# Kernel optimization log

Measured on AMD Instinct MI355X. Metric: run time of the kernel, lower is better.

Reference implementation:

```python
import jax, jax.numpy as jnp
import numpy as np

DIM_IN = 1024
DIM_OUT = 1024
B = 8192


def setup_inputs() -> dict:
    key = jax.random.key(0)
    ks = jax.random.split(key, 8)
    d = DIM_IN + DIM_OUT
    bound = 1.0 / np.sqrt(d)
    def lin(kw, kb):
        W = jax.random.uniform(kw, (d, DIM_OUT), jnp.float32, -bound, bound)
        b = jax.random.uniform(kb, (DIM_OUT,), jnp.float32, -bound, bound)
        return W, b
    kx, kh, kc, kp = ks[0], ks[1], ks[2], ks[3]
    pw = jax.random.split(kp, 8)
    W_I, b_I = lin(pw[0], pw[1])
    W_F, b_F = lin(pw[2], pw[3])
    W_G, b_G = lin(pw[4], pw[5])
    W_O, b_O = lin(pw[6], pw[7])
    return {
        "x": jax.random.normal(kx, (B, DIM_IN), jnp.float32),
        "h": jax.random.normal(kh, (B, DIM_OUT), jnp.float32),
        "c": jax.random.normal(kc, (B, DIM_OUT), jnp.float32),
        "W_I": W_I, "b_I": b_I,
        "W_F": W_F, "b_F": b_F,
        "W_G": W_G, "b_G": b_G,
        "W_O": W_O, "b_O": b_O,
    }


def reference(x, h, c, W_I, b_I, W_F, b_F, W_G, b_G, W_O, b_O):
    X = jnp.concatenate([x, h], axis=-1)  # [B, dimIn+dimOut]
    # Fuse the 4 gate projections into one GEMM: [B,d] @ [d, 4*dimOut]
    W = jnp.concatenate([W_I, W_F, W_G, W_O], axis=1)
    b = jnp.concatenate([b_I, b_F, b_G, b_O], axis=0)
    gates = X @ W + b
    i_, f_, g_, o_ = jnp.split(gates, 4, axis=-1)
    I = jax.nn.sigmoid(i_)
    F = jax.nn.sigmoid(f_)
    G = jnp.tanh(g_)
    O = jax.nn.sigmoid(o_)
    C = F * c + I * G
    return O * jnp.tanh(C), C
```

## Files before the change

kernel.cpp:

```cpp
#include <hip/hip_runtime.h>
#include <cstdint>


#define B_ROWS 8192
#define DK 2048
#define DOUT 1024
#define TM 128
#define TN 128
#define BK 32

typedef __bf16 bf16x8 __attribute__((ext_vector_type(8)));
typedef __bf16 bf16x4 __attribute__((ext_vector_type(4)));
typedef float f32x4 __attribute__((ext_vector_type(4)));

__device__ inline void load16_to_lds(const __bf16* gsrc, __bf16* ldst) {
    __builtin_amdgcn_global_load_lds(
        (const __attribute__((address_space(1))) void*)gsrc,
        (__attribute__((address_space(3))) void*)ldst,
        16, 0, 0);
}

__device__ inline float fast_sigmoid(float x) {
    return __builtin_amdgcn_rcpf(1.0f + __builtin_amdgcn_exp2f(-1.442695041f * x));
}
__device__ inline float fast_tanh(float x) {
    return 1.0f - 2.0f * __builtin_amdgcn_rcpf(1.0f + __builtin_amdgcn_exp2f(2.885390082f * x));
}

__global__ __launch_bounds__(256) void prep_x(const float* __restrict__ x,
                                              const float* __restrict__ h,
                                              __bf16* __restrict__ X) {
    int id = blockIdx.x * 256 + threadIdx.x;
    int b = id >> 9;
    int k = (id & 511) * 4;
    float4 v;
    if (k < 1024) v = *(const float4*)&x[(size_t)b * 1024 + k];
    else          v = *(const float4*)&h[(size_t)b * 1024 + (k - 1024)];
    bf16x4 o = { (__bf16)v.x, (__bf16)v.y, (__bf16)v.z, (__bf16)v.w };
    *(bf16x4*)&X[(size_t)b * 2048 + k] = o;
}

__global__ __launch_bounds__(256) void prep_w(const float* __restrict__ WI,
                                              const float* __restrict__ WF,
                                              const float* __restrict__ WG,
                                              const float* __restrict__ WO,
                                              __bf16* __restrict__ Wt) {
    int kb = blockIdx.x;
    int jb = blockIdx.y;
    int j0 = jb * 32;
    __shared__ float t[32][33];
    int tx = threadIdx.x, ty = threadIdx.y;
    const float* Ws[4] = {WI, WF, WG, WO};
#pragma unroll
    for (int g = 0; g < 4; ++g) {
        const float* W = Ws[g];
#pragma unroll
        for (int yy = 0; yy < 32; yy += 8) {
            int k = kb * 32 + ty + yy;
            t[ty + yy][tx] = W[(size_t)k * 1024 + j0 + tx];
        }
        __syncthreads();
#pragma unroll
        for (int yy = 0; yy < 32; yy += 8) {
            int r = ty + yy;
            int npp = (jb * 2 + (r >> 4)) * 64 + g * 16 + (r & 15);
            Wt[(size_t)npp * 2048 + kb * 32 + tx] = (__bf16)t[tx][r];
        }
        __syncthreads();
    }
}

__global__ __launch_bounds__(256) void lstm_gemm(
    const __bf16* __restrict__ Xbf, const __bf16* __restrict__ Wt,
    const float* __restrict__ c,
    const float* __restrict__ bI, const float* __restrict__ bF,
    const float* __restrict__ bG, const float* __restrict__ bO,
    float* __restrict__ outH, float* __restrict__ outC)
{
    __shared__ __bf16 As[TM * BK];
    __shared__ __bf16 Bs[TN * BK];

    const int t = threadIdx.x;
    const int lane = t & 63;
    const int wave = t >> 6;
    const int wm = wave >> 1;
    const int wn = wave & 1;
    const int m0 = blockIdx.x * TM;
    const int nb = blockIdx.y;
    const int n0 = nb * TN;

    f32x4 acc[4][4];
#pragma unroll
    for (int i = 0; i < 4; ++i)
#pragma unroll
        for (int j = 0; j < 4; ++j) acc[i][j] = (f32x4){0.f, 0.f, 0.f, 0.f};

    const int r0 = t >> 2, kc0 = (t & 3) * 8;
    const int r1 = 64 + r0;
    const __bf16* gA0 = Xbf + (size_t)(m0 + r0) * DK + kc0;
    const __bf16* gA1 = Xbf + (size_t)(m0 + r1) * DK + kc0;
    const __bf16* gB0 = Wt + (size_t)(n0 + r0) * DK + kc0;
    const __bf16* gB1 = Wt + (size_t)(n0 + r1) * DK + kc0;
    __bf16* lA0 = As + wave * 512;
    __bf16* lA1 = As + 2048 + wave * 512;
    __bf16* lB0 = Bs + wave * 512;
    __bf16* lB1 = Bs + 2048 + wave * 512;

    const int lr = lane & 15;
    const int kh = (lane >> 4) * 8;
    const int arow = wm * 64 + lr;
    const int brow = wn * 64 + lr;

    for (int kk = 0; kk < DK / BK; ++kk) {
        load16_to_lds(gA0, lA0);
        load16_to_lds(gA1, lA1);
        load16_to_lds(gB0, lB0);
        load16_to_lds(gB1, lB1);
        gA0 += BK; gA1 += BK; gB0 += BK; gB1 += BK;
        __syncthreads();

        bf16x8 a[4], b[4];
#pragma unroll
        for (int i = 0; i < 4; ++i)
            a[i] = *(const bf16x8*)&As[(arow + i * 16) * BK + kh];
#pragma unroll
        for (int j = 0; j < 4; ++j)
            b[j] = *(const bf16x8*)&Bs[(brow + j * 16) * BK + kh];
#pragma unroll
        for (int i = 0; i < 4; ++i)
#pragma unroll
            for (int j = 0; j < 4; ++j)
                acc[i][j] = __builtin_amdgcn_mfma_f32_16x16x32_bf16(a[i], b[j], acc[i][j], 0, 0, 0);
        __syncthreads();
    }

    const int col = lane & 15;
    const int j = (nb * 2 + wn) * 16 + col;
    const float biI = bI[j], biF = bF[j], biG = bG[j], biO = bO[j];
    const int rbase = m0 + wm * 64 + (lane >> 4) * 4;
#pragma unroll
    for (int i = 0; i < 4; ++i) {
#pragma unroll
        for (int r = 0; r < 4; ++r) {
            int row = rbase + i * 16 + r;
            float I = fast_sigmoid(acc[i][0][r] + biI);
            float F = fast_sigmoid(acc[i][1][r] + biF);
            float G = fast_tanh(acc[i][2][r] + biG);
            float O = fast_sigmoid(acc[i][3][r] + biO);
            size_t idx = (size_t)row * DOUT + j;
            float Cn = F * c[idx] + I * G;
            outH[idx] = O * fast_tanh(Cn);
            outC[idx] = Cn;
        }
    }
}

extern "C" void kernel_launch(void* const* d_in, const int* in_sizes, int n_in,
                              void* d_out, int out_size, void* d_ws, size_t ws_size,
                              hipStream_t stream) {
    const float* x  = (const float*)d_in[0];
    const float* h  = (const float*)d_in[1];
    const float* c  = (const float*)d_in[2];
    const float* WI = (const float*)d_in[3];
    const float* bI = (const float*)d_in[4];
    const float* WF = (const float*)d_in[5];
    const float* bF = (const float*)d_in[6];
    const float* WG = (const float*)d_in[7];
    const float* bG = (const float*)d_in[8];
    const float* WO = (const float*)d_in[9];
    const float* bO = (const float*)d_in[10];

    __bf16* Xbf = (__bf16*)d_ws;
    __bf16* Wt  = (__bf16*)((char*)d_ws + (size_t)B_ROWS * DK * 2);
    float* outH = (float*)d_out;
    float* outC = outH + (size_t)B_ROWS * DOUT;

    prep_x<<<(B_ROWS * DK / 4) / 256, 256, 0, stream>>>(x, h, Xbf);
    prep_w<<<dim3(DK / 32, DOUT / 32), dim3(32, 8), 0, stream>>>(WI, WF, WG, WO, Wt);
    lstm_gemm<<<dim3(B_ROWS / TM, 4 * DOUT / TN), 256, 0, stream>>>(
        Xbf, Wt, c, bI, bF, bG, bO, outH, outC);
}
```

Measured before the change: 359.6 us.

## Restructure LSTM GEMM into 256x256 double-buffered tiles with swizzled LDS

Rewrites the main GEMM to use 256x256 block tiles with 512 threads and a BK=64 K-step split into two halves. LDS is double-buffered so global-to-LDS loads for the next step overlap the MFMAs on the current one, using explicit waitcnt, barriers and setprio. The LDS layout is XOR-swizzled to avoid bank conflicts, and block IDs are remapped for better L2 locality. Each wave holds more accumulators (8x4), which raises register pressure and may reduce occupancy.

```diff
diff --git a/kernel.cpp b/kernel.cpp
--- a/kernel.cpp
+++ b/kernel.cpp
@@ -5,9 +5,10 @@
 #define B_ROWS 8192
 #define DK 2048
 #define DOUT 1024
-#define TM 128
-#define TN 128
-#define BK 32
+#define BM 256
+#define BN 256
+#define BK 64
+#define NKT (DK / BK)
 
 typedef __bf16 bf16x8 __attribute__((ext_vector_type(8)));
 typedef __bf16 bf16x4 __attribute__((ext_vector_type(4)));
@@ -70,83 +71,117 @@
     }
 }
 
-__global__ __launch_bounds__(256) void lstm_gemm(
+__global__ __launch_bounds__(512, 2) void lstm_gemm(
     const __bf16* __restrict__ Xbf, const __bf16* __restrict__ Wt,
     const float* __restrict__ c,
     const float* __restrict__ bI, const float* __restrict__ bF,
     const float* __restrict__ bG, const float* __restrict__ bO,
     float* __restrict__ outH, float* __restrict__ outC)
 {
-    __shared__ __bf16 As[TM * BK];
-    __shared__ __bf16 Bs[TN * BK];
-
-    const int t = threadIdx.x;
-    const int lane = t & 63;
-    const int wave = t >> 6;
-    const int wm = wave >> 1;
-    const int wn = wave & 1;
-    const int m0 = blockIdx.x * TM;
-    const int nb = blockIdx.y;
-    const int n0 = nb * TN;
-
-    f32x4 acc[4][4];
-#pragma unroll
-    for (int i = 0; i < 4; ++i)
-#pragma unroll
-        for (int j = 0; j < 4; ++j) acc[i][j] = (f32x4){0.f, 0.f, 0.f, 0.f};
-
-    const int r0 = t >> 2, kc0 = (t & 3) * 8;
-    const int r1 = 64 + r0;
-    const __bf16* gA0 = Xbf + (size_t)(m0 + r0) * DK + kc0;
-    const __bf16* gA1 = Xbf + (size_t)(m0 + r1) * DK + kc0;
-    const __bf16* gB0 = Wt + (size_t)(n0 + r0) * DK + kc0;
-    const __bf16* gB1 = Wt + (size_t)(n0 + r1) * DK + kc0;
-    __bf16* lA0 = As + wave * 512;
-    __bf16* lA1 = As + 2048 + wave * 512;
-    __bf16* lB0 = Bs + wave * 512;
-    __bf16* lB1 = Bs + 2048 + wave * 512;
+    __shared__ __bf16 lds[2][2][2][8192];
+
+    const int tid  = threadIdx.x;
+    const int lane = tid & 63;
+    const int wave = tid >> 6;
+    const int wm = wave >> 2;
+    const int wn = wave & 3;
+
+    const int bid = blockIdx.x;
+    const int id  = (bid & 7) * 64 + (bid >> 3);
+    const int mb = id & 31;
+    const int nb = id >> 5;
+    const int m0 = mb * BM;
+    const int n0 = nb * BN;
+
+    const int o0  = wave * 1024 + lane * 16;
+    const int r0  = o0 >> 6;
+    const int lc0 = ((o0 >> 4) & 3) ^ ((r0 >> 1) & 3);
+    const __bf16* gA0 = Xbf + (size_t)(m0 + r0)       * DK + lc0 * 8;
+    const __bf16* gA1 = Xbf + (size_t)(m0 + r0 + 128) * DK + lc0 * 8;
+    const __bf16* gB0 = Wt  + (size_t)(n0 + r0)       * DK + lc0 * 8;
+    const __bf16* gB1 = Wt  + (size_t)(n0 + r0 + 128) * DK + lc0 * 8;
+    const int ls0 = wave * 512;
+    const int ls1 = ls0 + 4096;
 
     const int lr = lane & 15;
-    const int kh = (lane >> 4) * 8;
-    const int arow = wm * 64 + lr;
-    const int brow = wn * 64 + lr;
-
-    for (int kk = 0; kk < DK / BK; ++kk) {
-        load16_to_lds(gA0, lA0);
-        load16_to_lds(gA1, lA1);
-        load16_to_lds(gB0, lB0);
-        load16_to_lds(gB1, lB1);
-        gA0 += BK; gA1 += BK; gB0 += BK; gB1 += BK;
-        __syncthreads();
-
-        bf16x8 a[4], b[4];
-#pragma unroll
-        for (int i = 0; i < 4; ++i)
-            a[i] = *(const bf16x8*)&As[(arow + i * 16) * BK + kh];
-#pragma unroll
-        for (int j = 0; j < 4; ++j)
-            b[j] = *(const bf16x8*)&Bs[(brow + j * 16) * BK + kh];
-#pragma unroll
-        for (int i = 0; i < 4; ++i)
-#pragma unroll
-            for (int j = 0; j < 4; ++j)
-                acc[i][j] = __builtin_amdgcn_mfma_f32_16x16x32_bf16(a[i], b[j], acc[i][j], 0, 0, 0);
-        __syncthreads();
+    const int pc = (lane >> 4) ^ ((lr >> 1) & 3);
+    const int ae = (wm * 128 + lr) * 32 + pc * 8;
+    const int be = (wn * 64  + lr) * 32 + pc * 8;
+
+    f32x4 acc[8][4];
+#pragma unroll
+    for (int i = 0; i < 8; ++i)
+#pragma unroll
+        for (int g = 0; g < 4; ++g) acc[i][g] = (f32x4){0.f, 0.f, 0.f, 0.f};
+
+#define STAGE_A(d_, kh_, ko_) do { \
+    load16_to_lds(gA0 + (ko_) + (kh_) * 32, &lds[d_][0][kh_][ls0]); \
+    load16_to_lds(gA1 + (ko_) + (kh_) * 32, &lds[d_][0][kh_][ls1]); } while (0)
+#define STAGE_B(d_, kh_, ko_) do { \
+    load16_to_lds(gB0 + (ko_) + (kh_) * 32, &lds[d_][1][kh_][ls0]); \
+    load16_to_lds(gB1 + (ko_) + (kh_) * 32, &lds[d_][1][kh_][ls1]); } while (0)
+
+    STAGE_A(0, 0, 0);
+    STAGE_B(0, 0, 0);
+    STAGE_A(0, 1, 0);
+    STAGE_B(0, 1, 0);
+
+#pragma unroll 2
+    for (int t = 0; t < NKT; ++t) {
+        const int d  = t & 1;
+        const int dn = d ^ 1;
+        const int ko = ((t + 1) & (NKT - 1)) * BK;
+#pragma unroll
+        for (int kh = 0; kh < 2; ++kh) {
+            asm volatile("s_waitcnt vmcnt(4) lgkmcnt(0)" ::: "memory");
+            __builtin_amdgcn_s_barrier();
+            asm volatile("" ::: "memory");
+            bf16x8 a[8], b0, b1;
+#pragma unroll
+            for (int mi = 0; mi < 8; ++mi)
+                a[mi] = *(const bf16x8*)&lds[d][0][kh][ae + mi * 512];
+            b0 = *(const bf16x8*)&lds[d][1][kh][be];
+            b1 = *(const bf16x8*)&lds[d][1][kh][be + 512];
+            STAGE_A(dn, kh, ko);
+            __builtin_amdgcn_s_setprio(1);
+#pragma unroll
+            for (int mi = 0; mi < 8; ++mi) {
+                acc[mi][0] = __builtin_amdgcn_mfma_f32_16x16x32_bf16(a[mi], b0, acc[mi][0], 0, 0, 0);
+                acc[mi][1] = __builtin_amdgcn_mfma_f32_16x16x32_bf16(a[mi], b1, acc[mi][1], 0, 0, 0);
+            }
+            __builtin_amdgcn_s_setprio(0);
+
+            asm volatile("s_waitcnt lgkmcnt(0)" ::: "memory");
+            __builtin_amdgcn_s_barrier();
+            asm volatile("" ::: "memory");
+            bf16x8 b2 = *(const bf16x8*)&lds[d][1][kh][be + 1024];
+            bf16x8 b3 = *(const bf16x8*)&lds[d][1][kh][be + 1536];
+            STAGE_B(dn, kh, ko);
+            __builtin_amdgcn_s_setprio(1);
+#pragma unroll
+            for (int mi = 0; mi < 8; ++mi) {
+                acc[mi][2] = __builtin_amdgcn_mfma_f32_16x16x32_bf16(a[mi], b2, acc[mi][2], 0, 0, 0);
+                acc[mi][3] = __builtin_amdgcn_mfma_f32_16x16x32_bf16(a[mi], b3, acc[mi][3], 0, 0, 0);
+            }
+            __builtin_amdgcn_s_setprio(0);
+        }
     }
+#undef STAGE_A
+#undef STAGE_B
 
     const int col = lane & 15;
-    const int j = (nb * 2 + wn) * 16 + col;
+    const int j = (nb * 4 + wn) * 16 + col;
     const float biI = bI[j], biF = bF[j], biG = bG[j], biO = bO[j];
-    const int rbase = m0 + wm * 64 + (lane >> 4) * 4;
-#pragma unroll
-    for (int i = 0; i < 4; ++i) {
+    const int rbase = m0 + wm * 128 + ((lane >> 4) << 2);
+#pragma unroll
+    for (int mi = 0; mi < 8; ++mi) {
 #pragma unroll
         for (int r = 0; r < 4; ++r) {
-            int row = rbase + i * 16 + r;
-            float I = fast_sigmoid(acc[i][0][r] + biI);
-            float F = fast_sigmoid(acc[i][1][r] + biF);
-            float G = fast_tanh(acc[i][2][r] + biG);
-            float O = fast_sigmoid(acc[i][3][r] + biO);
+            int row = rbase + mi * 16 + r;
+            float I = fast_sigmoid(acc[mi][0][r] + biI);
+            float F = fast_sigmoid(acc[mi][1][r] + biF);
+            float G = fast_tanh(acc[mi][2][r] + biG);
+            float O = fast_sigmoid(acc[mi][3][r] + biO);
             size_t idx = (size_t)row * DOUT + j;
             float Cn = F * c[idx] + I * G;
             outH[idx] = O * fast_tanh(Cn);
@@ -177,6 +212,6 @@
 
     prep_x<<<(B_ROWS * DK / 4) / 256, 256, 0, stream>>>(x, h, Xbf);
     prep_w<<<dim3(DK / 32, DOUT / 32), dim3(32, 8), 0, stream>>>(WI, WF, WG, WO, Wt);
-    lstm_gemm<<<dim3(B_ROWS / TM, 4 * DOUT / TN), 256, 0, stream>>>(
+    lstm_gemm<<<dim3((B_ROWS / BM) * (4 * DOUT / BN)), dim3(512), 0, stream>>>(
         Xbf, Wt, c, bI, bF, bG, bO, outH, outC);
 }
```

Result: faster. 311.9 us (-13.3%).
